# Performance work log

Measured on AMD Instinct MI355X. Metric: run time of the kernel, lower is better.

Reference implementation:

```python
import jax, jax.numpy as jnp
import numpy as np

B, D, H, T = 2048, 16, 256, 50
BETA_MIN, BETA_MAX = 0.1, 20.0


def setup_inputs() -> dict:
    key = jax.random.key(0)
    ks = jax.random.split(key, 6)
    s1 = 1.0 / np.sqrt(D)
    s2 = 1.0 / np.sqrt(H)
    return {
        "x": jax.random.normal(ks[0], (B, D), dtype=jnp.float32),
        "W1": jax.random.normal(ks[1], (D, H), dtype=jnp.float32) * s1,
        "b1": jnp.zeros((H,), dtype=jnp.float32),
        "wt": jax.random.normal(ks[2], (H,), dtype=jnp.float32) * 0.1,
        "W2": jax.random.normal(ks[3], (H, D), dtype=jnp.float32) * s2,
        "b2": jnp.zeros((D,), dtype=jnp.float32),
    }


def _dynamics(x, t, W1, b1, wt, W2, b2):
    # Reverse-time probability-flow ODE drift for a VP-SDE:
    #   dx/dt = f(x,t) - 0.5 * g(t)^2 * score(x,t)
    # with f = -0.5*beta(t)*x, g^2 = beta(t), score = MLP(x, t).
    beta = BETA_MIN + t * (BETA_MAX - BETA_MIN)
    h = jnp.tanh(x @ W1 + t * wt + b1)  # [B, H]
    score = h @ W2 + b2                 # [B, D]
    return -0.5 * beta * (x + score)


def _trace_jac(f, x):
    # Exact per-sample trace of the [D, D] Jacobian of f (batched over B)
    # via D forward-mode JVPs with basis tangents (batched, no per-output loop).
    eye = jnp.eye(x.shape[-1], dtype=x.dtype)

    def jvp_col(e):
        _, jv = jax.jvp(f, (x,), (jnp.broadcast_to(e, x.shape),))
        return jv  # [B, D]

    cols = jax.vmap(jvp_col)(eye)       # [D, B, D]
    return jnp.einsum("ibi->b", cols)   # sum of Jacobian diagonal per sample


def reference(x, W1, b1, wt, W2, b2):
    times = jnp.linspace(1e-3, 1.0, T, dtype=jnp.float32)

    def F(xc, t):
        dyn = lambda y: _dynamics(y, t, W1, b1, wt, W2, b2)
        dx = dyn(xc)
        tr = _trace_jac(dyn, xc)
        return dx, tr

    def rk4_step(carry, ts):
        xc, ldj = carry
        t0, t1 = ts
        h = t1 - t0
        k1x, k1t = F(xc, t0)
        k2x, k2t = F(xc + 0.5 * h * k1x, t0 + 0.5 * h)
        k3x, k3t = F(xc + 0.5 * h * k2x, t0 + 0.5 * h)
        k4x, k4t = F(xc + h * k3x, t1)
        xn = xc + (h / 6.0) * (k1x + 2.0 * k2x + 2.0 * k3x + k4x)
        ln = ldj + (h / 6.0) * (k1t + 2.0 * k2t + 2.0 * k3t + k4t)
        return (xn, ln), (xn, ln)

    ldj0 = jnp.zeros((x.shape[0],), dtype=x.dtype)
    (xf, ldjf), (xs, _) = jax.lax.scan(
        rk4_step, (x, ldj0), (times[:-1], times[1:])
    )
    xt = jnp.concatenate([x[None], xs], axis=0)  # [T, B, D] trajectory
    return xf, ldjf, xt
```

## Files before the change

kernel.cpp:

```cpp
#include <hip/hip_runtime.h>
#include <stdint.h>


typedef _Float16 f16x2 __attribute__((ext_vector_type(2)));

#if defined(__has_builtin)
#if __has_builtin(__builtin_amdgcn_fdot2)
#define HAVE_FDOT2 1
#endif
#endif

__device__ __forceinline__ float fdot2f(f16x2 a, f16x2 b, float c) {
#ifdef HAVE_FDOT2
    return __builtin_amdgcn_fdot2(a, b, c, false);
#else
    return fmaf((float)a.y, (float)b.y, fmaf((float)a.x, (float)b.x, c));
#endif
}

__device__ __forceinline__ uint32_t pk(float a, float b) {
    f16x2 v; v.x = (_Float16)a; v.y = (_Float16)b;
    return __builtin_bit_cast(uint32_t, v);
}
__device__ __forceinline__ f16x2 upk(uint32_t u) {
    return __builtin_bit_cast(f16x2, u);
}

#define Bn 2048
#define Dn 16
#define Hn 256
#define Tn 50
#define WPB 4
#define BLK (WPB * 64)
#define CHD 20

__global__ __launch_bounds__(BLK, 2) void ode_kernel(
    const float* __restrict__ x_in,
    const float* __restrict__ W1,
    const float* __restrict__ b1v,
    const float* __restrict__ wtv,
    const float* __restrict__ W2,
    const float* __restrict__ b2v,
    float* __restrict__ out)
{
    __shared__ __align__(16) uint32_t h_lds[WPB][8 * CHD];
    __shared__ __align__(16) uint32_t xe[WPB][12];

    const int t  = threadIdx.x;
    const int w  = t >> 6;
    const int L  = t & 63;
    const int g8 = L >> 3;
    const int c  = L & 7;
    const int ia = 2 * g8, ib = ia + 1;
    const int k0 = 4 * L;
    const int gs = blockIdx.x * WPB + w;

    f16x2 w1p[4][8];
    float b1k[4], wtk[4], ck[4];
    #pragma unroll
    for (int q = 0; q < 4; ++q) {
        #pragma unroll
        for (int j = 0; j < 8; ++j) {
            f16x2 v;
            v.x = (_Float16)W1[(2 * j)     * Hn + k0 + q];
            v.y = (_Float16)W1[(2 * j + 1) * Hn + k0 + q];
            w1p[q][j] = v;
        }
        b1k[q] = b1v[k0 + q];
        wtk[q] = wtv[k0 + q];
        float s = 0.f;
        #pragma unroll
        for (int ii = 0; ii < 16; ++ii)
            s = fmaf(W1[ii * Hn + k0 + q], W2[(k0 + q) * Dn + ii], s);
        ck[q] = s;
    }
    f16x2 w2a[16], w2b[16];
    #pragma unroll
    for (int m = 0; m < 16; ++m) {
        f16x2 va, vb;
        va.x = (_Float16)W2[(32 * c + 2 * m)     * Dn + ia];
        va.y = (_Float16)W2[(32 * c + 2 * m + 1) * Dn + ia];
        vb.x = (_Float16)W2[(32 * c + 2 * m)     * Dn + ib];
        vb.y = (_Float16)W2[(32 * c + 2 * m + 1) * Dn + ib];
        w2a[m] = va; w2b[m] = vb;
    }
    const float b2a = b2v[ia], b2b = b2v[ib];

    float xa = x_in[gs * Dn + ia];
    float xb = x_in[gs * Dn + ib];
    float ldjl = 0.f;

    float* xf_out  = out;
    float* ldj_out = out + (size_t)Bn * Dn;
    float* xt_ptr  = out + (size_t)Bn * Dn + Bn + gs * Dn + ia;

    if (c == 0) *(float2*)xt_ptr = make_float2(xa, xb);
    xt_ptr += Bn * Dn;

    auto Feval = [&](float xeva, float xevb, float tt, float wgt,
                     float& dxa, float& dxb) {
        if (c == 0) xe[w][g8] = pk(xeva, xevb);
        asm volatile("" ::: "memory");

        const uint4 xl0 = *(const uint4*)&xe[w][0];
        const uint4 xl1 = *(const uint4*)&xe[w][4];
        const f16x2 xp[8] = { upk(xl0.x), upk(xl0.y), upk(xl0.z), upk(xl0.w),
                              upk(xl1.x), upk(xl1.y), upk(xl1.z), upk(xl1.w) };
        float u0 = fmaf(tt, wtk[0], b1k[0]);
        float u1 = fmaf(tt, wtk[1], b1k[1]);
        float u2 = fmaf(tt, wtk[2], b1k[2]);
        float u3 = fmaf(tt, wtk[3], b1k[3]);
        #pragma unroll
        for (int j = 0; j < 8; ++j) {
            u0 = fdot2f(xp[j], w1p[0][j], u0);
            u1 = fdot2f(xp[j], w1p[1][j], u1);
            u2 = fdot2f(xp[j], w1p[2][j], u2);
            u3 = fdot2f(xp[j], w1p[3][j], u3);
        }
        const float h0 = fmaf(-2.f, __builtin_amdgcn_rcpf(__expf(2.f * u0) + 1.f), 1.f);
        const float h1 = fmaf(-2.f, __builtin_amdgcn_rcpf(__expf(2.f * u1) + 1.f), 1.f);
        const float h2 = fmaf(-2.f, __builtin_amdgcn_rcpf(__expf(2.f * u2) + 1.f), 1.f);
        const float h3 = fmaf(-2.f, __builtin_amdgcn_rcpf(__expf(2.f * u3) + 1.f), 1.f);

        const float gl = (fmaf(-h0 * h0, ck[0], ck[0]) + fmaf(-h1 * h1, ck[1], ck[1]))
                       + (fmaf(-h2 * h2, ck[2], ck[2]) + fmaf(-h3 * h3, ck[3], ck[3]));
        const float beta = fmaf(tt, 19.9f, 0.1f);
        const float nhb  = -0.5f * beta;
        ldjl = fmaf(wgt * nhb, 0.25f + gl, ldjl);

        *(uint2*)&h_lds[w][CHD * g8 + 2 * c] =
            make_uint2(pk(h0, h1), pk(h2, h3));
        asm volatile("" ::: "memory");

        float sa0 = 0.f, sa1 = 0.f, sb0 = 0.f, sb1 = 0.f;
        #pragma unroll
        for (int mq = 0; mq < 4; ++mq) {
            const uint4 hv = *(const uint4*)&h_lds[w][CHD * c + 4 * mq];
            const f16x2 p0 = upk(hv.x), p1 = upk(hv.y), p2 = upk(hv.z), p3 = upk(hv.w);
            sa0 = fdot2f(p0, w2a[4 * mq + 0], sa0);
            sb0 = fdot2f(p0, w2b[4 * mq + 0], sb0);
            sa1 = fdot2f(p1, w2a[4 * mq + 1], sa1);
            sb1 = fdot2f(p1, w2b[4 * mq + 1], sb1);
            sa0 = fdot2f(p2, w2a[4 * mq + 2], sa0);
            sb0 = fdot2f(p2, w2b[4 * mq + 2], sb0);
            sa1 = fdot2f(p3, w2a[4 * mq + 3], sa1);
            sb1 = fdot2f(p3, w2b[4 * mq + 3], sb1);
        }
        float sca = sa0 + sa1, scb = sb0 + sb1;
        sca += __shfl_xor(sca, 1);  scb += __shfl_xor(scb, 1);
        sca += __shfl_xor(sca, 2);  scb += __shfl_xor(scb, 2);
        sca += __shfl_xor(sca, 4);  scb += __shfl_xor(scb, 4);
        sca += b2a;  scb += b2b;

        dxa = nhb * (xeva + sca);
        dxb = nhb * (xevb + scb);
    };

    const float t_lo = 1e-3f;
    const float dt   = (1.0f - 1e-3f) / (float)(Tn - 1);

    for (int j = 0; j < Tn - 1; ++j) {
        const float t0 = fmaf((float)j,       dt, t_lo);
        const float t1 = fmaf((float)(j + 1), dt, t_lo);
        const float hh = t1 - t0;
        const float w1w = hh * (1.f / 6.f);
        const float w2w = hh * (2.f / 6.f);
        float k1a, k1b, k2a, k2b, k3a, k3b, k4a, k4b;
        Feval(xa, xb, t0, w1w, k1a, k1b);
        Feval(fmaf(0.5f * hh, k1a, xa), fmaf(0.5f * hh, k1b, xb),
              t0 + 0.5f * hh, w2w, k2a, k2b);
        Feval(fmaf(0.5f * hh, k2a, xa), fmaf(0.5f * hh, k2b, xb),
              t0 + 0.5f * hh, w2w, k3a, k3b);
        Feval(fmaf(hh, k3a, xa), fmaf(hh, k3b, xb),
              t1, w1w, k4a, k4b);
        xa = fmaf(w1w, k1a + 2.f * (k2a + k3a) + k4a, xa);
        xb = fmaf(w1w, k1b + 2.f * (k2b + k3b) + k4b, xb);
        if (c == 0) *(float2*)xt_ptr = make_float2(xa, xb);
        xt_ptr += Bn * Dn;
    }

    if (c == 0) *(float2*)(xf_out + gs * Dn + ia) = make_float2(xa, xb);

    #pragma unroll
    for (int off = 1; off < 64; off <<= 1)
        ldjl += __shfl_xor(ldjl, off);
    if (L == 0) ldj_out[gs] = ldjl;
}

extern "C" void kernel_launch(void* const* d_in, const int* in_sizes, int n_in,
                              void* d_out, int out_size, void* d_ws, size_t ws_size,
                              hipStream_t stream) {
    const float* x  = (const float*)d_in[0];
    const float* W1 = (const float*)d_in[1];
    const float* b1 = (const float*)d_in[2];
    const float* wt = (const float*)d_in[3];
    const float* W2 = (const float*)d_in[4];
    const float* b2 = (const float*)d_in[5];
    (void)in_sizes; (void)n_in; (void)out_size; (void)d_ws; (void)ws_size;
    ode_kernel<<<Bn / WPB, BLK, 0, stream>>>(x, W1, b1, wt, W2, b2, (float*)d_out);
}
```

Before: 199.6 us.

## Split each sample across two waves per block with block-level barriers

New measurement: 204.8 us. +2.6%, slower.

```diff
diff --git a/kernel.cpp b/kernel.cpp
--- a/kernel.cpp
+++ b/kernel.cpp
@@ -30,11 +30,10 @@
 #define Dn 16
 #define Hn 256
 #define Tn 50
-#define WPB 4
-#define BLK (WPB * 64)
-#define CHD 20
+#define BLK 128
+#define CH 20
 
-__global__ __launch_bounds__(BLK, 2) void ode_kernel(
+__global__ __launch_bounds__(BLK, 4) void ode_kernel(
     const float* __restrict__ x_in,
     const float* __restrict__ W1,
     const float* __restrict__ b1v,
@@ -43,148 +42,142 @@
     const float* __restrict__ b2v,
     float* __restrict__ out)
 {
-    __shared__ __align__(16) uint32_t h_lds[WPB][8 * CHD];
-    __shared__ __align__(16) uint32_t xe[WPB][12];
+    __shared__ __align__(16) uint32_t h_lds[8 * CH];
+    __shared__ __align__(16) _Float16 xe[16];
+    __shared__ float ldj_part[2];
 
-    const int t  = threadIdx.x;
-    const int w  = t >> 6;
-    const int L  = t & 63;
-    const int g8 = L >> 3;
-    const int c  = L & 7;
-    const int ia = 2 * g8, ib = ia + 1;
-    const int k0 = 4 * L;
-    const int gs = blockIdx.x * WPB + w;
+    const int t    = threadIdx.x;
+    const int W    = t >> 6;
+    const int L    = t & 63;
+    const int iloc = L >> 3;
+    const int c    = L & 7;
+    const int i    = 8 * W + iloc;
+    const int kp   = 64 * W + L;
+    const int gs   = blockIdx.x;
 
-    f16x2 w1p[4][8];
-    float b1k[4], wtk[4], ck[4];
+    f16x2 w1p[2][8];
+    float b1k[2], wtk[2], ck[2];
     #pragma unroll
-    for (int q = 0; q < 4; ++q) {
+    for (int q = 0; q < 2; ++q) {
+        const int k = 2 * kp + q;
         #pragma unroll
         for (int j = 0; j < 8; ++j) {
             f16x2 v;
-            v.x = (_Float16)W1[(2 * j)     * Hn + k0 + q];
-            v.y = (_Float16)W1[(2 * j + 1) * Hn + k0 + q];
+            v.x = (_Float16)W1[(2 * j)     * Hn + k];
+            v.y = (_Float16)W1[(2 * j + 1) * Hn + k];
             w1p[q][j] = v;
         }
-        b1k[q] = b1v[k0 + q];
-        wtk[q] = wtv[k0 + q];
+        b1k[q] = b1v[k];
+        wtk[q] = wtv[k];
         float s = 0.f;
         #pragma unroll
         for (int ii = 0; ii < 16; ++ii)
-            s = fmaf(W1[ii * Hn + k0 + q], W2[(k0 + q) * Dn + ii], s);
+            s = fmaf(W1[ii * Hn + k], W2[k * Dn + ii], s);
         ck[q] = s;
     }
-    f16x2 w2a[16], w2b[16];
+    f16x2 w2s[16];
     #pragma unroll
     for (int m = 0; m < 16; ++m) {
-        f16x2 va, vb;
-        va.x = (_Float16)W2[(32 * c + 2 * m)     * Dn + ia];
-        va.y = (_Float16)W2[(32 * c + 2 * m + 1) * Dn + ia];
-        vb.x = (_Float16)W2[(32 * c + 2 * m)     * Dn + ib];
-        vb.y = (_Float16)W2[(32 * c + 2 * m + 1) * Dn + ib];
-        w2a[m] = va; w2b[m] = vb;
+        f16x2 v;
+        v.x = (_Float16)W2[(32 * c + 2 * m)     * Dn + i];
+        v.y = (_Float16)W2[(32 * c + 2 * m + 1) * Dn + i];
+        w2s[m] = v;
     }
-    const float b2a = b2v[ia], b2b = b2v[ib];
+    const float b2i = b2v[i];
 
-    float xa = x_in[gs * Dn + ia];
-    float xb = x_in[gs * Dn + ib];
+    float x    = x_in[gs * Dn + i];
     float ldjl = 0.f;
 
     float* xf_out  = out;
     float* ldj_out = out + (size_t)Bn * Dn;
-    float* xt_ptr  = out + (size_t)Bn * Dn + Bn + gs * Dn + ia;
+    float* xt_base = out + (size_t)Bn * Dn + Bn + gs * Dn + i;
 
-    if (c == 0) *(float2*)xt_ptr = make_float2(xa, xb);
-    xt_ptr += Bn * Dn;
+    if (c == 0) xt_base[0] = x;
 
-    auto Feval = [&](float xeva, float xevb, float tt, float wgt,
-                     float& dxa, float& dxb) {
-        if (c == 0) xe[w][g8] = pk(xeva, xevb);
-        asm volatile("" ::: "memory");
+    const int hwidx = CH * (kp >> 4) + (kp & 15);
 
-        const uint4 xl0 = *(const uint4*)&xe[w][0];
-        const uint4 xl1 = *(const uint4*)&xe[w][4];
+    auto Feval = [&](float xev, float tt, float wgt) -> float {
+        const uint4 xl0 = *(const uint4*)&xe[0];
+        const uint4 xl1 = *(const uint4*)&xe[8];
         const f16x2 xp[8] = { upk(xl0.x), upk(xl0.y), upk(xl0.z), upk(xl0.w),
                               upk(xl1.x), upk(xl1.y), upk(xl1.z), upk(xl1.w) };
         float u0 = fmaf(tt, wtk[0], b1k[0]);
         float u1 = fmaf(tt, wtk[1], b1k[1]);
-        float u2 = fmaf(tt, wtk[2], b1k[2]);
-        float u3 = fmaf(tt, wtk[3], b1k[3]);
         #pragma unroll
         for (int j = 0; j < 8; ++j) {
             u0 = fdot2f(xp[j], w1p[0][j], u0);
             u1 = fdot2f(xp[j], w1p[1][j], u1);
-            u2 = fdot2f(xp[j], w1p[2][j], u2);
-            u3 = fdot2f(xp[j], w1p[3][j], u3);
         }
         const float h0 = fmaf(-2.f, __builtin_amdgcn_rcpf(__expf(2.f * u0) + 1.f), 1.f);
         const float h1 = fmaf(-2.f, __builtin_amdgcn_rcpf(__expf(2.f * u1) + 1.f), 1.f);
-        const float h2 = fmaf(-2.f, __builtin_amdgcn_rcpf(__expf(2.f * u2) + 1.f), 1.f);
-        const float h3 = fmaf(-2.f, __builtin_amdgcn_rcpf(__expf(2.f * u3) + 1.f), 1.f);
+        h_lds[hwidx] = pk(h0, h1);
 
-        const float gl = (fmaf(-h0 * h0, ck[0], ck[0]) + fmaf(-h1 * h1, ck[1], ck[1]))
-                       + (fmaf(-h2 * h2, ck[2], ck[2]) + fmaf(-h3 * h3, ck[3], ck[3]));
+        const float gl = fmaf(-h0 * h0, ck[0], ck[0]) + fmaf(-h1 * h1, ck[1], ck[1]);
         const float beta = fmaf(tt, 19.9f, 0.1f);
         const float nhb  = -0.5f * beta;
-        ldjl = fmaf(wgt * nhb, 0.25f + gl, ldjl);
+        ldjl = fmaf(wgt * nhb, 0.125f + gl, ldjl);
 
-        *(uint2*)&h_lds[w][CHD * g8 + 2 * c] =
-            make_uint2(pk(h0, h1), pk(h2, h3));
-        asm volatile("" ::: "memory");
+        __syncthreads();
 
-        float sa0 = 0.f, sa1 = 0.f, sb0 = 0.f, sb1 = 0.f;
+        float s0 = 0.f, s1 = 0.f;
         #pragma unroll
         for (int mq = 0; mq < 4; ++mq) {
-            const uint4 hv = *(const uint4*)&h_lds[w][CHD * c + 4 * mq];
-            const f16x2 p0 = upk(hv.x), p1 = upk(hv.y), p2 = upk(hv.z), p3 = upk(hv.w);
-            sa0 = fdot2f(p0, w2a[4 * mq + 0], sa0);
-            sb0 = fdot2f(p0, w2b[4 * mq + 0], sb0);
-            sa1 = fdot2f(p1, w2a[4 * mq + 1], sa1);
-            sb1 = fdot2f(p1, w2b[4 * mq + 1], sb1);
-            sa0 = fdot2f(p2, w2a[4 * mq + 2], sa0);
-            sb0 = fdot2f(p2, w2b[4 * mq + 2], sb0);
-            sa1 = fdot2f(p3, w2a[4 * mq + 3], sa1);
-            sb1 = fdot2f(p3, w2b[4 * mq + 3], sb1);
+            const uint4 hv = *(const uint4*)&h_lds[CH * c + 4 * mq];
+            s0 = fdot2f(upk(hv.x), w2s[4 * mq + 0], s0);
+            s1 = fdot2f(upk(hv.y), w2s[4 * mq + 1], s1);
+            s0 = fdot2f(upk(hv.z), w2s[4 * mq + 2], s0);
+            s1 = fdot2f(upk(hv.w), w2s[4 * mq + 3], s1);
         }
-        float sca = sa0 + sa1, scb = sb0 + sb1;
-        sca += __shfl_xor(sca, 1);  scb += __shfl_xor(scb, 1);
-        sca += __shfl_xor(sca, 2);  scb += __shfl_xor(scb, 2);
-        sca += __shfl_xor(sca, 4);  scb += __shfl_xor(scb, 4);
-        sca += b2a;  scb += b2b;
+        float sc = s0 + s1;
+        sc += __shfl_xor(sc, 1);
+        sc += __shfl_xor(sc, 2);
+        sc += __shfl_xor(sc, 4);
+        sc += b2i;
+        return nhb * (xev + sc);
+    };
 
-        dxa = nhb * (xeva + sca);
-        dxb = nhb * (xevb + scb);
+    auto put_xe = [&](float v) {
+        if (c == 0) xe[i] = (_Float16)v;
     };
 
     const float t_lo = 1e-3f;
     const float dt   = (1.0f - 1e-3f) / (float)(Tn - 1);
 
+    put_xe(x);
+    __syncthreads();
+
     for (int j = 0; j < Tn - 1; ++j) {
-        const float t0 = fmaf((float)j,       dt, t_lo);
-        const float t1 = fmaf((float)(j + 1), dt, t_lo);
-        const float hh = t1 - t0;
+        const float t0  = fmaf((float)j,       dt, t_lo);
+        const float t1  = fmaf((float)(j + 1), dt, t_lo);
+        const float hh  = t1 - t0;
+        const float tm  = t0 + 0.5f * hh;
         const float w1w = hh * (1.f / 6.f);
         const float w2w = hh * (2.f / 6.f);
-        float k1a, k1b, k2a, k2b, k3a, k3b, k4a, k4b;
-        Feval(xa, xb, t0, w1w, k1a, k1b);
-        Feval(fmaf(0.5f * hh, k1a, xa), fmaf(0.5f * hh, k1b, xb),
-              t0 + 0.5f * hh, w2w, k2a, k2b);
-        Feval(fmaf(0.5f * hh, k2a, xa), fmaf(0.5f * hh, k2b, xb),
-              t0 + 0.5f * hh, w2w, k3a, k3b);
-        Feval(fmaf(hh, k3a, xa), fmaf(hh, k3b, xb),
-              t1, w1w, k4a, k4b);
-        xa = fmaf(w1w, k1a + 2.f * (k2a + k3a) + k4a, xa);
-        xb = fmaf(w1w, k1b + 2.f * (k2b + k3b) + k4b, xb);
-        if (c == 0) *(float2*)xt_ptr = make_float2(xa, xb);
-        xt_ptr += Bn * Dn;
+
+        const float k1 = Feval(x, t0, w1w);
+        const float e2 = fmaf(0.5f * hh, k1, x);
+        put_xe(e2); __syncthreads();
+        const float k2 = Feval(e2, tm, w2w);
+        const float e3 = fmaf(0.5f * hh, k2, x);
+        put_xe(e3); __syncthreads();
+        const float k3 = Feval(e3, tm, w2w);
+        const float e4 = fmaf(hh, k3, x);
+        put_xe(e4); __syncthreads();
+        const float k4 = Feval(e4, t1, w1w);
+
+        x = fmaf(w1w, k1 + 2.f * (k2 + k3) + k4, x);
+        if (c == 0) xt_base[(size_t)(j + 1) * (Bn * Dn)] = x;
+        put_xe(x); __syncthreads();
     }
 
-    if (c == 0) *(float2*)(xf_out + gs * Dn + ia) = make_float2(xa, xb);
+    if (c == 0) xf_out[gs * Dn + i] = x;
 
     #pragma unroll
     for (int off = 1; off < 64; off <<= 1)
         ldjl += __shfl_xor(ldjl, off);
-    if (L == 0) ldj_out[gs] = ldjl;
+    if (L == 0) ldj_part[W] = ldjl;
+    __syncthreads();
+    if (t == 0) ldj_out[gs] = ldj_part[0] + ldj_part[1];
 }
 
 extern "C" void kernel_launch(void* const* d_in, const int* in_sizes, int n_in,
@@ -197,5 +190,5 @@
     const float* W2 = (const float*)d_in[4];
     const float* b2 = (const float*)d_in[5];
     (void)in_sizes; (void)n_in; (void)out_size; (void)d_ws; (void)ws_size;
-    ode_kernel<<<Bn / WPB, BLK, 0, stream>>>(x, W1, b1, wt, W2, b2, (float*)d_out);
+    ode_kernel<<<Bn, BLK, 0, stream>>>(x, W1, b1, wt, W2, b2, (float*)d_out);
 }
```

## Use one wave per block, readlane broadcast, DPP reductions, and exp2 tanh

Applied to the files above, without the earlier changes.

New measurement: 171.6 us. 14.0% less time.

```diff
diff --git a/kernel.cpp b/kernel.cpp
--- a/kernel.cpp
+++ b/kernel.cpp
@@ -26,15 +26,23 @@
     return __builtin_bit_cast(f16x2, u);
 }
 
+#define DPP_XOR1 0xB1
+#define DPP_XOR2 0x4E
+#define DPP_RHM  0x141
+template <int CTRL>
+__device__ __forceinline__ float dpp_add(float x) {
+    int v = __builtin_amdgcn_update_dpp(
+        0, __builtin_bit_cast(int, x), CTRL, 0xF, 0xF, true);
+    return x + __builtin_bit_cast(float, v);
+}
+
 #define Bn 2048
 #define Dn 16
 #define Hn 256
 #define Tn 50
-#define WPB 4
-#define BLK (WPB * 64)
-#define CHD 20
-
-__global__ __launch_bounds__(BLK, 2) void ode_kernel(
+#define CH 20
+
+__global__ __launch_bounds__(64) void ode_kernel(
     const float* __restrict__ x_in,
     const float* __restrict__ W1,
     const float* __restrict__ b1v,
@@ -43,35 +51,35 @@
     const float* __restrict__ b2v,
     float* __restrict__ out)
 {
-    __shared__ __align__(16) uint32_t h_lds[WPB][8 * CHD];
-    __shared__ __align__(16) uint32_t xe[WPB][12];
-
-    const int t  = threadIdx.x;
-    const int w  = t >> 6;
-    const int L  = t & 63;
+    __shared__ __align__(16) uint32_t h_lds[8 * CH];
+
+    const int L  = threadIdx.x;
     const int g8 = L >> 3;
     const int c  = L & 7;
     const int ia = 2 * g8, ib = ia + 1;
     const int k0 = 4 * L;
-    const int gs = blockIdx.x * WPB + w;
+    const int gs = blockIdx.x;
+
+    const float K2 = 2.88539008f;
 
     f16x2 w1p[4][8];
     float b1k[4], wtk[4], ck[4];
     #pragma unroll
     for (int q = 0; q < 4; ++q) {
+        const int k = k0 + q;
         #pragma unroll
         for (int j = 0; j < 8; ++j) {
             f16x2 v;
-            v.x = (_Float16)W1[(2 * j)     * Hn + k0 + q];
-            v.y = (_Float16)W1[(2 * j + 1) * Hn + k0 + q];
+            v.x = (_Float16)(K2 * W1[(2 * j)     * Hn + k]);
+            v.y = (_Float16)(K2 * W1[(2 * j + 1) * Hn + k]);
             w1p[q][j] = v;
         }
-        b1k[q] = b1v[k0 + q];
-        wtk[q] = wtv[k0 + q];
+        b1k[q] = K2 * b1v[k];
+        wtk[q] = K2 * wtv[k];
         float s = 0.f;
         #pragma unroll
         for (int ii = 0; ii < 16; ++ii)
-            s = fmaf(W1[ii * Hn + k0 + q], W2[(k0 + q) * Dn + ii], s);
+            s = fmaf(W1[ii * Hn + k], W2[k * Dn + ii], s);
         ck[q] = s;
     }
     f16x2 w2a[16], w2b[16];
@@ -88,7 +96,8 @@
 
     float xa = x_in[gs * Dn + ia];
     float xb = x_in[gs * Dn + ib];
-    float ldjl = 0.f;
+    float ldjl  = 0.f;
+    float wbsum = 0.f;
 
     float* xf_out  = out;
     float* ldj_out = out + (size_t)Bn * Dn;
@@ -97,15 +106,25 @@
     if (c == 0) *(float2*)xt_ptr = make_float2(xa, xb);
     xt_ptr += Bn * Dn;
 
+    const int hwidx = CH * (L >> 3) + 2 * (L & 7);
+
+    uint32_t se0, se1, se2, se3, se4, se5, se6, se7;
+    auto bcast = [&](float ea, float eb) {
+        const uint32_t vpk = pk(ea, eb);
+        se0 = __builtin_amdgcn_readlane(vpk,  0);
+        se1 = __builtin_amdgcn_readlane(vpk,  8);
+        se2 = __builtin_amdgcn_readlane(vpk, 16);
+        se3 = __builtin_amdgcn_readlane(vpk, 24);
+        se4 = __builtin_amdgcn_readlane(vpk, 32);
+        se5 = __builtin_amdgcn_readlane(vpk, 40);
+        se6 = __builtin_amdgcn_readlane(vpk, 48);
+        se7 = __builtin_amdgcn_readlane(vpk, 56);
+    };
+
     auto Feval = [&](float xeva, float xevb, float tt, float wgt,
                      float& dxa, float& dxb) {
-        if (c == 0) xe[w][g8] = pk(xeva, xevb);
-        asm volatile("" ::: "memory");
-
-        const uint4 xl0 = *(const uint4*)&xe[w][0];
-        const uint4 xl1 = *(const uint4*)&xe[w][4];
-        const f16x2 xp[8] = { upk(xl0.x), upk(xl0.y), upk(xl0.z), upk(xl0.w),
-                              upk(xl1.x), upk(xl1.y), upk(xl1.z), upk(xl1.w) };
+        const f16x2 xp[8] = { upk(se0), upk(se1), upk(se2), upk(se3),
+                              upk(se4), upk(se5), upk(se6), upk(se7) };
         float u0 = fmaf(tt, wtk[0], b1k[0]);
         float u1 = fmaf(tt, wtk[1], b1k[1]);
         float u2 = fmaf(tt, wtk[2], b1k[2]);
@@ -117,25 +136,26 @@
             u2 = fdot2f(xp[j], w1p[2][j], u2);
             u3 = fdot2f(xp[j], w1p[3][j], u3);
         }
-        const float h0 = fmaf(-2.f, __builtin_amdgcn_rcpf(__expf(2.f * u0) + 1.f), 1.f);
-        const float h1 = fmaf(-2.f, __builtin_amdgcn_rcpf(__expf(2.f * u1) + 1.f), 1.f);
-        const float h2 = fmaf(-2.f, __builtin_amdgcn_rcpf(__expf(2.f * u2) + 1.f), 1.f);
-        const float h3 = fmaf(-2.f, __builtin_amdgcn_rcpf(__expf(2.f * u3) + 1.f), 1.f);
+        const float h0 = fmaf(-2.f, __builtin_amdgcn_rcpf(__builtin_amdgcn_exp2f(u0) + 1.f), 1.f);
+        const float h1 = fmaf(-2.f, __builtin_amdgcn_rcpf(__builtin_amdgcn_exp2f(u1) + 1.f), 1.f);
+        const float h2 = fmaf(-2.f, __builtin_amdgcn_rcpf(__builtin_amdgcn_exp2f(u2) + 1.f), 1.f);
+        const float h3 = fmaf(-2.f, __builtin_amdgcn_rcpf(__builtin_amdgcn_exp2f(u3) + 1.f), 1.f);
+        *(uint2*)&h_lds[hwidx] = make_uint2(pk(h0, h1), pk(h2, h3));
 
         const float gl = (fmaf(-h0 * h0, ck[0], ck[0]) + fmaf(-h1 * h1, ck[1], ck[1]))
                        + (fmaf(-h2 * h2, ck[2], ck[2]) + fmaf(-h3 * h3, ck[3], ck[3]));
         const float beta = fmaf(tt, 19.9f, 0.1f);
         const float nhb  = -0.5f * beta;
-        ldjl = fmaf(wgt * nhb, 0.25f + gl, ldjl);
-
-        *(uint2*)&h_lds[w][CHD * g8 + 2 * c] =
-            make_uint2(pk(h0, h1), pk(h2, h3));
+        const float wb   = wgt * nhb;
+        ldjl  = fmaf(wb, gl, ldjl);
+        wbsum += wb;
+
         asm volatile("" ::: "memory");
 
         float sa0 = 0.f, sa1 = 0.f, sb0 = 0.f, sb1 = 0.f;
         #pragma unroll
         for (int mq = 0; mq < 4; ++mq) {
-            const uint4 hv = *(const uint4*)&h_lds[w][CHD * c + 4 * mq];
+            const uint4 hv = *(const uint4*)&h_lds[CH * c + 4 * mq];
             const f16x2 p0 = upk(hv.x), p1 = upk(hv.y), p2 = upk(hv.z), p3 = upk(hv.w);
             sa0 = fdot2f(p0, w2a[4 * mq + 0], sa0);
             sb0 = fdot2f(p0, w2b[4 * mq + 0], sb0);
@@ -147,9 +167,9 @@
             sb1 = fdot2f(p3, w2b[4 * mq + 3], sb1);
         }
         float sca = sa0 + sa1, scb = sb0 + sb1;
-        sca += __shfl_xor(sca, 1);  scb += __shfl_xor(scb, 1);
-        sca += __shfl_xor(sca, 2);  scb += __shfl_xor(scb, 2);
-        sca += __shfl_xor(sca, 4);  scb += __shfl_xor(scb, 4);
+        sca = dpp_add<DPP_XOR1>(sca);  scb = dpp_add<DPP_XOR1>(scb);
+        sca = dpp_add<DPP_XOR2>(sca);  scb = dpp_add<DPP_XOR2>(scb);
+        sca = dpp_add<DPP_RHM >(sca);  scb = dpp_add<DPP_RHM >(scb);
         sca += b2a;  scb += b2b;
 
         dxa = nhb * (xeva + sca);
@@ -158,29 +178,41 @@
 
     const float t_lo = 1e-3f;
     const float dt   = (1.0f - 1e-3f) / (float)(Tn - 1);
-
+    const float hh   = dt;
+    const float w1w  = hh * (1.f / 6.f);
+    const float w2w  = hh * (2.f / 6.f);
+
+    bcast(xa, xb);
     for (int j = 0; j < Tn - 1; ++j) {
-        const float t0 = fmaf((float)j,       dt, t_lo);
-        const float t1 = fmaf((float)(j + 1), dt, t_lo);
-        const float hh = t1 - t0;
-        const float w1w = hh * (1.f / 6.f);
-        const float w2w = hh * (2.f / 6.f);
+        const float t0 = fmaf((float)j, dt, t_lo);
+        const float tm = t0 + 0.5f * hh;
+        const float t1 = t0 + hh;
         float k1a, k1b, k2a, k2b, k3a, k3b, k4a, k4b;
+
         Feval(xa, xb, t0, w1w, k1a, k1b);
-        Feval(fmaf(0.5f * hh, k1a, xa), fmaf(0.5f * hh, k1b, xb),
-              t0 + 0.5f * hh, w2w, k2a, k2b);
-        Feval(fmaf(0.5f * hh, k2a, xa), fmaf(0.5f * hh, k2b, xb),
-              t0 + 0.5f * hh, w2w, k3a, k3b);
-        Feval(fmaf(hh, k3a, xa), fmaf(hh, k3b, xb),
-              t1, w1w, k4a, k4b);
+        const float e2a = fmaf(0.5f * hh, k1a, xa);
+        const float e2b = fmaf(0.5f * hh, k1b, xb);
+        bcast(e2a, e2b);
+        Feval(e2a, e2b, tm, w2w, k2a, k2b);
+        const float e3a = fmaf(0.5f * hh, k2a, xa);
+        const float e3b = fmaf(0.5f * hh, k2b, xb);
+        bcast(e3a, e3b);
+        Feval(e3a, e3b, tm, w2w, k3a, k3b);
+        const float e4a = fmaf(hh, k3a, xa);
+        const float e4b = fmaf(hh, k3b, xb);
+        bcast(e4a, e4b);
+        Feval(e4a, e4b, t1, w1w, k4a, k4b);
+
         xa = fmaf(w1w, k1a + 2.f * (k2a + k3a) + k4a, xa);
         xb = fmaf(w1w, k1b + 2.f * (k2b + k3b) + k4b, xb);
         if (c == 0) *(float2*)xt_ptr = make_float2(xa, xb);
         xt_ptr += Bn * Dn;
+        bcast(xa, xb);
     }
 
     if (c == 0) *(float2*)(xf_out + gs * Dn + ia) = make_float2(xa, xb);
 
+    ldjl = fmaf(0.25f, wbsum, ldjl);
     #pragma unroll
     for (int off = 1; off < 64; off <<= 1)
         ldjl += __shfl_xor(ldjl, off);
@@ -197,5 +229,5 @@
     const float* W2 = (const float*)d_in[4];
     const float* b2 = (const float*)d_in[5];
     (void)in_sizes; (void)n_in; (void)out_size; (void)d_ws; (void)ws_size;
-    ode_kernel<<<Bn / WPB, BLK, 0, stream>>>(x, W1, b1, wt, W2, b2, (float*)d_out);
-}
+    ode_kernel<<<Bn, 64, 0, stream>>>(x, W1, b1, wt, W2, b2, (float*)d_out);
+}
```
